# Performance work log

Measured on AMD Instinct MI355X. Metric: run time of the kernel, lower is better.

## Reference

```python
import jax, jax.numpy as jnp
import numpy as np

B, C, N = 512, 4, 24
D, H, L, DFF = 512, 8, 4, 2048
D2, D4 = D // 2, D // 4


def _ln(x, g, b):
    m = x.mean(-1, keepdims=True)
    v = ((x - m) ** 2).mean(-1, keepdims=True)
    return (x - m) / jnp.sqrt(v + 1e-5) * g + b


def setup_inputs():
    key = jax.random.key(0)
    ks = iter(jax.random.split(key, 80))
    def glorot(shape):
        fi, fo = shape[-2], shape[-1]
        return jax.random.normal(next(ks), shape, jnp.float32) * np.float32(np.sqrt(2.0 / (fi + fo)))
    z = lambda shape: jnp.zeros(shape, jnp.float32)
    o = lambda shape: jnp.ones(shape, jnp.float32)
    inp = {
        'encoded_features': jax.random.normal(next(ks), (B, C, D), jnp.float32),
        'original_keypoints': jax.random.normal(next(ks), (B, C, N, 2), jnp.float32),
        'depth_map': jax.random.uniform(next(ks), (B, C, N), jnp.float32),
        'occlusion_mask': jax.random.bernoulli(next(ks), 0.7, (B, C, N)),
        'kp_emb': jax.random.normal(next(ks), (N, D), jnp.float32) * 0.02,
        'view_emb': jax.random.normal(next(ks), (C, D), jnp.float32) * 0.02,
        'Wq': glorot((L, D, D)), 'bq': z((L, D)),
        'Wk': glorot((L, D, D)), 'bk': z((L, D)),
        'Wv': glorot((L, D, D)), 'bv': z((L, D)),
        'Wo': glorot((L, D, D)), 'bo': z((L, D)),
        'ln1_g': o((L, D)), 'ln1_b': z((L, D)),
        'ln2_g': o((L, D)), 'ln2_b': z((L, D)),
        'ffn_w1': glorot((L, D, DFF)), 'ffn_b1': z((L, DFF)),
        'ffn_w2': glorot((L, DFF, D)), 'ffn_b2': z((L, D)),
        'pred_w1': glorot((D, D2)), 'pred_b1': z((D2,)),
        'pred_w2': glorot((D2, D4)), 'pred_b2': z((D4,)),
        'pred_w3': glorot((D4, 2)), 'pred_b3': z((2,)),
        'de_w1': glorot((1, D4)), 'de_b1': z((D4,)),
        'de_w2': glorot((D4, D2)), 'de_b2': z((D2,)),
        'mp_w': glorot((D + D2, D)), 'mp_b': z((D,)),
        'dp_w1': glorot((D, D2)), 'dp_b1': z((D2,)),
        'dp_w2': glorot((D2, D4)), 'dp_b2': z((D4,)),
        'dp_w3': glorot((D4, 1)), 'dp_b3': z((1,)),
        'conf_w': glorot((D, 1)), 'conf_b': z((1,)),
    }
    return inp


def _forward(encoded_features, original_keypoints, depth_map, kp_emb, view_emb,
             Wq, bq, Wk, bk, Wv, bv, Wo, bo, ln1_g, ln1_b, ln2_g, ln2_b,
             ffn_w1, ffn_b1, ffn_w2, ffn_b2, pred_w1, pred_b1, pred_w2, pred_b2,
             pred_w3, pred_b3, de_w1, de_b1, de_w2, de_b2, mp_w, mp_b,
             dp_w1, dp_b1, dp_w2, dp_b2, dp_w3, dp_b3, conf_w, conf_b,
             occlusion_mask):
    occluded = ~occlusion_mask  # (B,C,N) True = needs inpainting
    # Vectorized replacement for the nested B*C ragged depth loop:
    # encode every depth scalar, masked mean over visible keypoints per (b,c).
    d_enc = jax.nn.gelu(depth_map[..., None] @ de_w1 + de_b1) @ de_w2 + de_b2  # (B,C,N,D2)
    vis = occlusion_mask[..., None].astype(jnp.float32)
    cnt = vis.sum(2)  # (B,C,1)
    depth_feat = jnp.where(cnt > 0, (d_enc * vis).sum(2) / jnp.maximum(cnt, 1.0), 0.0)
    # NOTE: faithful to source — `memory` is projected but the attention layers
    # consume encoded_features directly, so this is dead w.r.t. outputs.
    _memory = jnp.concatenate([encoded_features, depth_feat], -1) @ mp_w + mp_b

    # Dense query set over all (c,n); occluded positions selected at the end
    # (same math as the nonzero/gather version, jit-friendly fixed shapes).
    q = (view_emb[:, None, :] + kp_emb[None, :, :]).reshape(1, C * N, D)
    q = jnp.broadcast_to(q, (B, C * N, D))
    mem = encoded_features  # (B,C,D)
    dh = D // H
    scale = np.float32(1.0 / np.sqrt(dh))
    for l in range(L):  # post-LN cross-attention block (assumed standard block)
        qh = (q @ Wq[l] + bq[l]).reshape(B, C * N, H, dh)
        kh = (mem @ Wk[l] + bk[l]).reshape(B, C, H, dh)
        vh = (mem @ Wv[l] + bv[l]).reshape(B, C, H, dh)
        att = jax.nn.softmax(jnp.einsum('bqhd,bkhd->bhqk', qh, kh) * scale, axis=-1)
        attn_out = jnp.einsum('bhqk,bkhd->bqhd', att, vh).reshape(B, C * N, D) @ Wo[l] + bo[l]
        q = _ln(q + attn_out, ln1_g[l], ln1_b[l])
        f = jax.nn.gelu(q @ ffn_w1[l] + ffn_b1[l]) @ ffn_w2[l] + ffn_b2[l]
        q = _ln(q + f, ln2_g[l], ln2_b[l])

    feat = q  # (B, C*N, D)
    pred = jax.nn.gelu(feat @ pred_w1 + pred_b1)
    pred = jax.nn.gelu(pred @ pred_w2 + pred_b2) @ pred_w3 + pred_b3  # (B,CN,2)
    coords = jnp.where(occluded[..., None], pred.reshape(B, C, N, 2), original_keypoints)
    conf = jnp.where(occluded, jax.nn.sigmoid(feat @ conf_w + conf_b).reshape(B, C, N), 0.0)
    dp = jax.nn.gelu(feat @ dp_w1 + dp_b1)
    dp = jax.nn.softplus(jax.nn.gelu(dp @ dp_w2 + dp_b2) @ dp_w3 + dp_b3)
    depth = jnp.where(occluded, dp.reshape(B, C, N), 0.0)
    return coords, conf, depth


def reference(encoded_features, original_keypoints, depth_map, kp_emb, view_emb,
              Wq, bq, Wk, bk, Wv, bv, Wo, bo, ln1_g, ln1_b, ln2_g, ln2_b,
              ffn_w1, ffn_b1, ffn_w2, ffn_b2, pred_w1, pred_b1, pred_w2, pred_b2,
              pred_w3, pred_b3, de_w1, de_b1, de_w2, de_b2, mp_w, mp_b,
              dp_w1, dp_b1, dp_w2, dp_b2, dp_w3, dp_b3, conf_w, conf_b,
              occlusion_mask):
    return _forward(encoded_features, original_keypoints, depth_map, kp_emb, view_emb,
                    Wq, bq, Wk, bk, Wv, bv, Wo, bo, ln1_g, ln1_b, ln2_g, ln2_b,
                    ffn_w1, ffn_b1, ffn_w2, ffn_b2, pred_w1, pred_b1, pred_w2, pred_b2,
                    pred_w3, pred_b3, de_w1, de_b1, de_w2, de_b2, mp_w, mp_b,
                    dp_w1, dp_b1, dp_w2, dp_b2, dp_w3, dp_b3, conf_w, conf_b,
                    occlusion_mask)
```

## Files before the change

kernel.cpp:

```cpp
#include <hip/hip_runtime.h>
#include <hip/hip_bf16.h>
#include <stdint.h>

using bf16 = __hip_bfloat16;
typedef __attribute__((ext_vector_type(8))) short short8;
typedef __attribute__((ext_vector_type(4))) float f32x4;

#define GLD16(gptr, lptr) \
  __builtin_amdgcn_global_load_lds((const __attribute__((address_space(1))) void*)(gptr), \
                                   (__attribute__((address_space(3))) void*)(lptr), 16, 0, 0)

#define BARRIER_FENCED() do { \
  __builtin_amdgcn_s_barrier(); \
  asm volatile("" ::: "memory"); \
  __builtin_amdgcn_sched_barrier(0); \
} while (0)

__device__ __forceinline__ float b2f(bf16 h){ return __bfloat162float(h); }
__device__ __forceinline__ bf16  f2b(float f){ return __float2bfloat16(f); }
__device__ __forceinline__ float geluf(float x){
  float t2 = 1.5957691216057308f * (x + 0.044715f*x*x*x);
  return x / (1.0f + __expf(-t2));
}
__device__ __forceinline__ float wsum(float v){
  v += __shfl_xor(v,32); v += __shfl_xor(v,16); v += __shfl_xor(v,8);
  v += __shfl_xor(v,4);  v += __shfl_xor(v,2);  v += __shfl_xor(v,1);
  return v;
}

union BV { uint4 u; bf16 h[8]; };

template<int EPI>
__global__ __launch_bounds__(256, 2)
void gemm_bt(const bf16* __restrict__ A, int lda,
             const bf16* __restrict__ Bt,
             const float* __restrict__ bias,
             bf16* __restrict__ C, int ldc, int K)
{
  __shared__ __align__(16) bf16 smem[32768];
  const int tid  = threadIdx.x;
  const int wave = tid >> 6;
  const int lane = tid & 63;

  const int nwg = gridDim.x * gridDim.y;
  int bid = blockIdx.x + gridDim.x * blockIdx.y;
  if ((nwg & 7) == 0) bid = (bid & 7) * (nwg >> 3) + (bid >> 3);
  const int bx = bid % gridDim.x;
  const int by = bid / gridDim.x;
  const long mBlk = (long)by * 128;
  const int  nBlk = bx * 128;
  const int wm = (wave >> 1) * 64;
  const int wn = (wave & 1)  * 64;

  const int lr = lane >> 3;
  const int kc = ((lane & 7) ^ lr) << 3;
  const bf16* aS = A  + (mBlk + wave*32 + lr) * (long)lda + kc;
  const bf16* bS = Bt + (long)(nBlk + wave*32 + lr) * K   + kc;

  const int sA = lane >> 4;
  const int rA = wm + (lane & 15);
  const int rB = wn + (lane & 15);
  const int xA = rA & 7, xB = rB & 7;

  f32x4 acc[4][4];
  #pragma unroll
  for (int m=0;m<4;++m)
    #pragma unroll
    for (int n=0;n<4;++n)
      acc[m][n] = (f32x4){0.f,0.f,0.f,0.f};

  auto STAGE = [&](int b, int t) {
    bf16* sAl = smem + b*16384 + wave*2048;
    bf16* sBl = smem + b*16384 + 8192 + wave*2048;
    const int ko = t*64;
    #pragma unroll
    for (int c=0;c<4;++c) {
      GLD16(aS + (long)c*8*lda + ko, sAl + c*512);
      GLD16(bS + (long)c*8*K   + ko, sBl + c*512);
    }
  };
  auto COMPUTE = [&](int b) {
    const bf16* s = smem + b*16384;
    #pragma unroll
    for (int ks=0; ks<2; ++ks) {
      const int j = (ks<<2) + sA;
      short8 af[4], bfv[4];
      #pragma unroll
      for (int m=0;m<4;++m)
        af[m]  = *(const short8*)&s[(rA + m*16)*64 + ((j ^ xA) << 3)];
      #pragma unroll
      for (int n=0;n<4;++n)
        bfv[n] = *(const short8*)&s[8192 + (rB + n*16)*64 + ((j ^ xB) << 3)];
      #pragma unroll
      for (int m=0;m<4;++m)
        #pragma unroll
        for (int n=0;n<4;++n)
          acc[m][n] = __builtin_amdgcn_mfma_f32_16x16x32_bf16(af[m], bfv[n], acc[m][n], 0, 0, 0);
    }
  };

  STAGE(0, 0);
  asm volatile("s_waitcnt vmcnt(0)" ::: "memory");
  BARRIER_FENCED();

  const int nt = K >> 6;
  int cur = 0;
  for (int t = 0; t < nt - 1; ++t) {
    STAGE(cur ^ 1, t + 1);
    COMPUTE(cur);
    asm volatile("s_waitcnt vmcnt(0)" ::: "memory");
    BARRIER_FENCED();
    cur ^= 1;
  }
  COMPUTE(cur);

  __syncthreads();
  #pragma unroll
  for (int n=0;n<4;++n) {
    const int col = wn + n*16 + (lane & 15);
    float bi = bias[nBlk + col];
    #pragma unroll
    for (int m=0;m<4;++m) {
      #pragma unroll
      for (int j=0;j<4;++j) {
        float x = acc[m][n][j] + bi;
        if (EPI == 1) x = geluf(x);
        smem[(wm + m*16 + (lane>>4)*4 + j)*136 + col] = f2b(x);
      }
    }
  }
  __syncthreads();
  #pragma unroll
  for (int it=0; it<8; ++it) {
    int o = it*2048 + tid*8;
    int row = o >> 7, col = o & 127;
    uint4 v = *(const uint4*)&smem[row*136 + col];
    *(uint4*)&C[(mBlk + row)*(long)ldc + nBlk + col] = v;
  }
}

__global__ void transpose_w(const float* __restrict__ src, bf16* __restrict__ dst,
                            int N, long srcStride, long dstStride, int dstRowOff, int dstLd)
{
  __shared__ float t[32][33];
  src += (long)blockIdx.z * srcStride;
  dst += (long)blockIdx.z * dstStride;
  int n0 = blockIdx.x*32, k0 = blockIdx.y*32;
  int tx = threadIdx.x & 31, ty = threadIdx.x >> 5;
  #pragma unroll
  for (int r=0;r<4;++r) t[ty + r*8][tx] = src[(long)(k0+ty+r*8)*N + n0+tx];
  __syncthreads();
  #pragma unroll
  for (int r=0;r<4;++r)
    dst[(long)(dstRowOff + n0 + ty + r*8)*dstLd + k0 + tx] = f2b(t[tx][ty+r*8]);
}

__global__ void f32_to_bf16_k(const float* __restrict__ src, bf16* __restrict__ dst, long n)
{
  long i = ((long)blockIdx.x*256 + threadIdx.x) * 4;
  if (i + 3 < n) {
    float4 v = *(const float4*)(src + i);
    dst[i+0]=f2b(v.x); dst[i+1]=f2b(v.y); dst[i+2]=f2b(v.z); dst[i+3]=f2b(v.w);
  }
}

__global__ void concat2(float* __restrict__ dst, long dStride,
                        const float* __restrict__ a, long aStride, int na,
                        const float* __restrict__ b, long bStride, int nb)
{
  int z = blockIdx.y;
  int i = blockIdx.x*256 + threadIdx.x;
  if (i < na) dst[z*dStride + i] = a[z*aStride + i];
  else if (i < na + nb) dst[z*dStride + i] = b[z*bStride + (i - na)];
}

__global__ void init_q(const float* __restrict__ vw, const float* __restrict__ kp,
                       bf16* __restrict__ q)
{
  long gid = (long)blockIdx.x*256 + threadIdx.x;
  int b  = (int)(gid / 6144);
  int r  = (int)(gid % 6144);
  int cn = r >> 6;
  int d0 = (r & 63) * 8;
  int c = cn / 24, n = cn % 24;
  const float4* v4 = (const float4*)(vw + c*512 + d0);
  const float4* k4 = (const float4*)(kp + n*512 + d0);
  float4 va = v4[0], vb = v4[1], ka = k4[0], kb = k4[1];
  BV o;
  o.h[0]=f2b(va.x+ka.x); o.h[1]=f2b(va.y+ka.y); o.h[2]=f2b(va.z+ka.z); o.h[3]=f2b(va.w+ka.w);
  o.h[4]=f2b(vb.x+kb.x); o.h[5]=f2b(vb.y+kb.y); o.h[6]=f2b(vb.z+kb.z); o.h[7]=f2b(vb.w+kb.w);
  *(uint4*)(q + (long)b*49152 + cn*512 + d0) = o.u;
}

__global__ void add_ln(bf16* __restrict__ q, const bf16* __restrict__ res,
                       const float* __restrict__ g, const float* __restrict__ b)
{
  int row  = blockIdx.x*4 + (threadIdx.x >> 6);
  int lane = threadIdx.x & 63;
  long o = (long)row*512 + lane*8;
  BV Q, R;
  Q.u = *(const uint4*)(q + o);
  R.u = *(const uint4*)(res + o);
  float s[8]; float sum=0.f, sq=0.f;
  #pragma unroll
  for (int j=0;j<8;++j){ s[j] = b2f(Q.h[j]) + b2f(R.h[j]); sum += s[j]; sq += s[j]*s[j]; }
  sum = wsum(sum); sq = wsum(sq);
  float mean = sum * 0.001953125f;
  float var  = sq  * 0.001953125f - mean*mean;
  float rstd = rsqrtf(var + 1e-5f);
  const float4* g4 = (const float4*)(g + lane*8);
  const float4* b4 = (const float4*)(b + lane*8);
  float4 g0=g4[0], g1=g4[1], b0=b4[0], b1=b4[1];
  float gg[8] = {g0.x,g0.y,g0.z,g0.w,g1.x,g1.y,g1.z,g1.w};
  float bb[8] = {b0.x,b0.y,b0.z,b0.w,b1.x,b1.y,b1.z,b1.w};
  BV O;
  #pragma unroll
  for (int j=0;j<8;++j) O.h[j] = f2b((s[j]-mean)*rstd*gg[j] + bb[j]);
  *(uint4*)(q + o) = O.u;
}

__global__ void attn_k(bf16* __restrict__ qh, const bf16* __restrict__ kvh)
{
  int row  = blockIdx.x*4 + (threadIdx.x >> 6);
  int lane = threadIdx.x & 63;
  int b = row / 96;
  int d = (lane >> 3)*64 + (lane & 7)*8;
  BV Q;
  Q.u = *(const uint4*)(qh + (long)row*512 + d);
  float qf[8];
  #pragma unroll
  for (int j=0;j<8;++j) qf[j] = b2f(Q.h[j]);
  float s[4];
  #pragma unroll
  for (int c=0;c<4;++c){
    BV K; K.u = *(const uint4*)(kvh + (long)(b*4+c)*1024 + d);
    float p = 0.f;
    #pragma unroll
    for (int j=0;j<8;++j) p += qf[j]*b2f(K.h[j]);
    p += __shfl_xor(p,1); p += __shfl_xor(p,2); p += __shfl_xor(p,4);
    s[c] = p * 0.125f;
  }
  float mx = fmaxf(fmaxf(s[0],s[1]), fmaxf(s[2],s[3]));
  float e0=expf(s[0]-mx), e1=expf(s[1]-mx), e2=expf(s[2]-mx), e3=expf(s[3]-mx);
  float inv = 1.f/(e0+e1+e2+e3);
  float p4[4] = {e0*inv, e1*inv, e2*inv, e3*inv};
  float o[8] = {0,0,0,0,0,0,0,0};
  #pragma unroll
  for (int c=0;c<4;++c){
    BV V; V.u = *(const uint4*)(kvh + (long)(b*4+c)*1024 + 512 + d);
    #pragma unroll
    for (int j=0;j<8;++j) o[j] += p4[c]*b2f(V.h[j]);
  }
  BV O;
  #pragma unroll
  for (int j=0;j<8;++j) O.h[j] = f2b(o[j]);
  *(uint4*)(qh + (long)row*512 + d) = O.u;
}

__global__ void finalize_k(const bf16* __restrict__ feat, const bf16* __restrict__ p2dp2,
                           const float* __restrict__ cw, const float* __restrict__ cb,
                           const float* __restrict__ pw3, const float* __restrict__ pb3,
                           const float* __restrict__ dw3, const float* __restrict__ db3,
                           const int* __restrict__ occ, const float* __restrict__ okp,
                           float* __restrict__ out)
{
  int row  = blockIdx.x*4 + (threadIdx.x >> 6);
  int lane = threadIdx.x & 63;
  BV F; F.u = *(const uint4*)(feat + (long)row*512 + lane*8);
  const float4* c4 = (const float4*)(cw + lane*8);
  float4 ca = c4[0], cbv = c4[1];
  float cwv[8] = {ca.x,ca.y,ca.z,ca.w,cbv.x,cbv.y,cbv.z,cbv.w};
  float pc = 0.f;
  #pragma unroll
  for (int j=0;j<8;++j) pc += b2f(F.h[j]) * cwv[j];
  float sc = wsum(pc);
  int k = lane*2;
  long o2 = (long)row*256;
  float a0 = b2f(p2dp2[o2 + k]),       a1 = b2f(p2dp2[o2 + k + 1]);
  float d0 = b2f(p2dp2[o2 + 128 + k]), d1 = b2f(p2dp2[o2 + 128 + k + 1]);
  float sx = a0*pw3[k*2]   + a1*pw3[(k+1)*2];
  float sy = a0*pw3[k*2+1] + a1*pw3[(k+1)*2+1];
  float sd = d0*dw3[k]     + d1*dw3[k+1];
  sx = wsum(sx); sy = wsum(sy); sd = wsum(sd);
  if (lane == 0) {
    bool occl = (occ[row] == 0);
    out[row*2]   = occl ? (sx + pb3[0]) : okp[row*2];
    out[row*2+1] = occl ? (sy + pb3[1]) : okp[row*2+1];
    out[98304 + row] = occl ? 1.f/(1.f + expf(-(sc + cb[0]))) : 0.f;
    float dd = sd + db3[0];
    float sp = fmaxf(dd, 0.f) + log1pf(expf(-fabsf(dd)));
    out[147456 + row] = occl ? sp : 0.f;
  }
}

extern "C" void kernel_launch(void* const* d_in, const int* in_sizes, int n_in,
                              void* d_out, int out_size, void* d_ws, size_t ws_size,
                              hipStream_t stream)
{
  const float* enc  = (const float*)d_in[0];
  const float* okp  = (const float*)d_in[1];
  const int*   occ  = (const int*)  d_in[3];
  const float* kp   = (const float*)d_in[4];
  const float* vw   = (const float*)d_in[5];
  const float* Wq   = (const float*)d_in[6];
  const float* bq   = (const float*)d_in[7];
  const float* Wk   = (const float*)d_in[8];
  const float* bk   = (const float*)d_in[9];
  const float* Wv   = (const float*)d_in[10];
  const float* bv   = (const float*)d_in[11];
  const float* Wo   = (const float*)d_in[12];
  const float* bo   = (const float*)d_in[13];
  const float* ln1g = (const float*)d_in[14];
  const float* ln1b = (const float*)d_in[15];
  const float* ln2g = (const float*)d_in[16];
  const float* ln2b = (const float*)d_in[17];
  const float* fw1  = (const float*)d_in[18];
  const float* fb1  = (const float*)d_in[19];
  const float* fw2  = (const float*)d_in[20];
  const float* fb2  = (const float*)d_in[21];
  const float* pw1  = (const float*)d_in[22];
  const float* pb1  = (const float*)d_in[23];
  const float* pw2  = (const float*)d_in[24];
  const float* pb2  = (const float*)d_in[25];
  const float* pw3  = (const float*)d_in[26];
  const float* pb3  = (const float*)d_in[27];
  const float* dw1  = (const float*)d_in[34];
  const float* db1  = (const float*)d_in[35];
  const float* dw2  = (const float*)d_in[36];
  const float* db2  = (const float*)d_in[37];
  const float* dw3  = (const float*)d_in[38];
  const float* db3  = (const float*)d_in[39];
  const float* cw   = (const float*)d_in[40];
  const float* cb   = (const float*)d_in[41];

  uint8_t* base = (uint8_t*)d_ws;
  size_t off = 0;
  auto alloc = [&](size_t bytes) -> void* {
    void* p = base + off;
    off = (off + bytes + 255) & ~(size_t)255;
    return p;
  };
  bf16*  wqT  = (bf16*) alloc(4ull*512*512*2);
  bf16*  kvT  = (bf16*) alloc(4ull*1024*512*2);
  bf16*  woT  = (bf16*) alloc(4ull*512*512*2);
  bf16*  w1T  = (bf16*) alloc(4ull*2048*512*2);
  bf16*  w2T  = (bf16*) alloc(4ull*512*2048*2);
  bf16*  pd1T = (bf16*) alloc(512ull*512*2);
  bf16*  pw2T = (bf16*) alloc(128ull*256*2);
  bf16*  dw2T = (bf16*) alloc(128ull*256*2);
  float* bkvb = (float*)alloc(4ull*1024*4);
  float* pd1b = (float*)alloc(512ull*4);
  bf16*  mem16= (bf16*) alloc(2048ull*512*2);
  bf16*  kv16 = (bf16*) alloc(2048ull*1024*2);
  bf16*  q16  = (bf16*) alloc(49152ull*512*2);
  bf16*  bufQH= (bf16*) alloc(49152ull*512*2);
  size_t remainB = (ws_size > off) ? (ws_size - off) : 0;
  int chunkRows;
  if      (remainB >= 16384ull*2048*2 + 512) chunkRows = 16384;
  else if (remainB >= 12288ull*2048*2 + 512) chunkRows = 12288;
  else                                        chunkRows = 6144;
  bf16*  bufF1= (bf16*) alloc((size_t)chunkRows*2048*2);
  if (off > ws_size) return;
  const int nCh = 49152 / chunkRows;
  long woRows = (long)chunkRows * 4;
  if (woRows > 49152) woRows = 49152;
  const int nWo = (int)(49152 / woRows);

  dim3 T(256);
  transpose_w<<<dim3(16,16,4), T, 0, stream>>>(Wq,  wqT, 512, 512*512, 512*512, 0, 512);
  transpose_w<<<dim3(16,16,4), T, 0, stream>>>(Wk,  kvT, 512, 512*512, 1024*512, 0, 512);
  transpose_w<<<dim3(16,16,4), T, 0, stream>>>(Wv,  kvT, 512, 512*512, 1024*512, 512, 512);
  transpose_w<<<dim3(16,16,4), T, 0, stream>>>(Wo,  woT, 512, 512*512, 512*512, 0, 512);
  transpose_w<<<dim3(64,16,4), T, 0, stream>>>(fw1, w1T, 2048, 512*2048, 2048*512, 0, 512);
  transpose_w<<<dim3(16,64,4), T, 0, stream>>>(fw2, w2T, 512, 2048*512, 512*2048, 0, 2048);
  transpose_w<<<dim3(8,16,1),  T, 0, stream>>>(pw1, pd1T, 256, 0, 0, 0,   512);
  transpose_w<<<dim3(8,16,1),  T, 0, stream>>>(dw1, pd1T, 256, 0, 0, 256, 512);
  transpose_w<<<dim3(4,8,1),   T, 0, stream>>>(pw2, pw2T, 128, 0, 0, 0, 256);
  transpose_w<<<dim3(4,8,1),   T, 0, stream>>>(dw2, dw2T, 128, 0, 0, 0, 256);
  concat2<<<dim3(4,4), T, 0, stream>>>(bkvb, 1024, bk, 512, 512, bv, 512, 512);
  concat2<<<dim3(2,1), T, 0, stream>>>(pd1b, 512, pb1, 256, 256, db1, 256, 256);
  f32_to_bf16_k<<<dim3(1024), T, 0, stream>>>(enc, mem16, 2048ll*512);
  init_q<<<dim3(12288), T, 0, stream>>>(vw, kp, q16);

  for (int l = 0; l < 4; ++l) {
    gemm_bt<0><<<dim3(4,384), T, 0, stream>>>(q16, 512, wqT + l*262144, bq + l*512, bufQH, 512, 512);
    gemm_bt<0><<<dim3(8,16),  T, 0, stream>>>(mem16, 512, kvT + l*524288, bkvb + l*1024, kv16, 1024, 512);
    attn_k<<<dim3(12288), T, 0, stream>>>(bufQH, kv16);
    for (int c = 0; c < nWo; ++c) {
      gemm_bt<0><<<dim3(4, (int)(woRows>>7)), T, 0, stream>>>(bufQH + (long)c*woRows*512, 512,
                                                woT + l*262144, bo + l*512, bufF1, 512, 512);
      add_ln<<<dim3((int)(woRows>>2)), T, 0, stream>>>(q16 + (long)c*woRows*512, bufF1,
                                           ln1g + l*512, ln1b + l*512);
    }
    for (int c = 0; c < nCh; ++c) {
      gemm_bt<1><<<dim3(16, chunkRows>>7), T, 0, stream>>>(q16 + (long)c*chunkRows*512, 512,
                                                w1T + l*1048576, fb1 + l*2048, bufF1, 2048, 512);
      gemm_bt<0><<<dim3(4, chunkRows>>7),  T, 0, stream>>>(bufF1, 2048,
                                                w2T + l*1048576, fb2 + l*512,
                                                bufQH + (long)c*chunkRows*512, 512, 2048);
      add_ln<<<dim3(chunkRows>>2), T, 0, stream>>>(q16 + (long)c*chunkRows*512,
                                           bufQH + (long)c*chunkRows*512,
                                           ln2g + l*512, ln2b + l*512);
    }
  }

  gemm_bt<1><<<dim3(4,384), T, 0, stream>>>(q16, 512, pd1T, pd1b, bufQH, 512, 512);
  gemm_bt<1><<<dim3(1,384), T, 0, stream>>>(bufQH, 512, pw2T, pb2, bufF1, 256, 256);
  gemm_bt<1><<<dim3(1,384), T, 0, stream>>>(bufQH + 256, 512, dw2T, db2, bufF1 + 128, 256, 256);
  finalize_k<<<dim3(12288), T, 0, stream>>>(q16, bufF1, cw, cb, pw3, pb3, dw3, db3,
                                            occ, okp, (float*)d_out);
}
```

Before: 1.711 ms.

## Single-buffer GEMM for higher occupancy; dedupe layer-0 Q projection across batch

```diff
diff --git a/kernel.cpp b/kernel.cpp
--- a/kernel.cpp
+++ b/kernel.cpp
@@ -9,12 +9,6 @@
 #define GLD16(gptr, lptr) \
   __builtin_amdgcn_global_load_lds((const __attribute__((address_space(1))) void*)(gptr), \
                                    (__attribute__((address_space(3))) void*)(lptr), 16, 0, 0)
-
-#define BARRIER_FENCED() do { \
-  __builtin_amdgcn_s_barrier(); \
-  asm volatile("" ::: "memory"); \
-  __builtin_amdgcn_sched_barrier(0); \
-} while (0)
 
 __device__ __forceinline__ float b2f(bf16 h){ return __bfloat162float(h); }
 __device__ __forceinline__ bf16  f2b(float f){ return __float2bfloat16(f); }
@@ -31,13 +25,13 @@
 union BV { uint4 u; bf16 h[8]; };
 
 template<int EPI>
-__global__ __launch_bounds__(256, 2)
+__global__ __launch_bounds__(256, 4)
 void gemm_bt(const bf16* __restrict__ A, int lda,
              const bf16* __restrict__ Bt,
              const float* __restrict__ bias,
              bf16* __restrict__ C, int ldc, int K)
 {
-  __shared__ __align__(16) bf16 smem[32768];
+  __shared__ __align__(16) bf16 smem[17408];
   const int tid  = threadIdx.x;
   const int wave = tid >> 6;
   const int lane = tid & 63;
@@ -69,52 +63,38 @@
     for (int n=0;n<4;++n)
       acc[m][n] = (f32x4){0.f,0.f,0.f,0.f};
 
-  auto STAGE = [&](int b, int t) {
-    bf16* sAl = smem + b*16384 + wave*2048;
-    bf16* sBl = smem + b*16384 + 8192 + wave*2048;
-    const int ko = t*64;
-    #pragma unroll
-    for (int c=0;c<4;++c) {
-      GLD16(aS + (long)c*8*lda + ko, sAl + c*512);
-      GLD16(bS + (long)c*8*K   + ko, sBl + c*512);
-    }
-  };
-  auto COMPUTE = [&](int b) {
-    const bf16* s = smem + b*16384;
+  const int nt = K >> 6;
+  for (int t = 0; t < nt; ++t) {
+    {
+      bf16* sAl = smem + wave*2048;
+      bf16* sBl = smem + 8192 + wave*2048;
+      const int ko = t*64;
+      #pragma unroll
+      for (int c=0;c<4;++c) {
+        GLD16(aS + (long)c*8*lda + ko, sAl + c*512);
+        GLD16(bS + (long)c*8*K   + ko, sBl + c*512);
+      }
+    }
+    __syncthreads();
     #pragma unroll
     for (int ks=0; ks<2; ++ks) {
       const int j = (ks<<2) + sA;
       short8 af[4], bfv[4];
       #pragma unroll
       for (int m=0;m<4;++m)
-        af[m]  = *(const short8*)&s[(rA + m*16)*64 + ((j ^ xA) << 3)];
+        af[m]  = *(const short8*)&smem[(rA + m*16)*64 + ((j ^ xA) << 3)];
       #pragma unroll
       for (int n=0;n<4;++n)
-        bfv[n] = *(const short8*)&s[8192 + (rB + n*16)*64 + ((j ^ xB) << 3)];
+        bfv[n] = *(const short8*)&smem[8192 + (rB + n*16)*64 + ((j ^ xB) << 3)];
       #pragma unroll
       for (int m=0;m<4;++m)
         #pragma unroll
         for (int n=0;n<4;++n)
           acc[m][n] = __builtin_amdgcn_mfma_f32_16x16x32_bf16(af[m], bfv[n], acc[m][n], 0, 0, 0);
     }
-  };
-
-  STAGE(0, 0);
-  asm volatile("s_waitcnt vmcnt(0)" ::: "memory");
-  BARRIER_FENCED();
-
-  const int nt = K >> 6;
-  int cur = 0;
-  for (int t = 0; t < nt - 1; ++t) {
-    STAGE(cur ^ 1, t + 1);
-    COMPUTE(cur);
-    asm volatile("s_waitcnt vmcnt(0)" ::: "memory");
-    BARRIER_FENCED();
-    cur ^= 1;
-  }
-  COMPUTE(cur);
-
-  __syncthreads();
+    __syncthreads();
+  }
+
   #pragma unroll
   for (int n=0;n<4;++n) {
     const int col = wn + n*16 + (lane & 15);
@@ -192,6 +172,22 @@
   *(uint4*)(q + (long)b*49152 + cn*512 + d0) = o.u;
 }
 
+__global__ void init_q96(const float* __restrict__ vw, const float* __restrict__ kp,
+                         bf16* __restrict__ q96)
+{
+  int gid = blockIdx.x*256 + threadIdx.x;
+  int cn = gid >> 6;
+  int d0 = (gid & 63) * 8;
+  int c = cn / 24, n = cn % 24;
+  const float4* v4 = (const float4*)(vw + c*512 + d0);
+  const float4* k4 = (const float4*)(kp + n*512 + d0);
+  float4 va = v4[0], vb = v4[1], ka = k4[0], kb = k4[1];
+  BV o;
+  o.h[0]=f2b(va.x+ka.x); o.h[1]=f2b(va.y+ka.y); o.h[2]=f2b(va.z+ka.z); o.h[3]=f2b(va.w+ka.w);
+  o.h[4]=f2b(vb.x+kb.x); o.h[5]=f2b(vb.y+kb.y); o.h[6]=f2b(vb.z+kb.z); o.h[7]=f2b(vb.w+kb.w);
+  *(uint4*)(q96 + (long)cn*512 + d0) = o.u;
+}
+
 __global__ void add_ln(bf16* __restrict__ q, const bf16* __restrict__ res,
                        const float* __restrict__ g, const float* __restrict__ b)
 {
@@ -219,14 +215,16 @@
   *(uint4*)(q + o) = O.u;
 }
 
-__global__ void attn_k(bf16* __restrict__ qh, const bf16* __restrict__ kvh)
+__global__ void attn_k(const bf16* __restrict__ qsrc, int qMod,
+                       const bf16* __restrict__ kvh, bf16* __restrict__ dst)
 {
   int row  = blockIdx.x*4 + (threadIdx.x >> 6);
   int lane = threadIdx.x & 63;
   int b = row / 96;
+  int qRow = qMod ? (row % qMod) : row;
   int d = (lane >> 3)*64 + (lane & 7)*8;
   BV Q;
-  Q.u = *(const uint4*)(qh + (long)row*512 + d);
+  Q.u = *(const uint4*)(qsrc + (long)qRow*512 + d);
   float qf[8];
   #pragma unroll
   for (int j=0;j<8;++j) qf[j] = b2f(Q.h[j]);
@@ -254,7 +252,7 @@
   BV O;
   #pragma unroll
   for (int j=0;j<8;++j) O.h[j] = f2b(o[j]);
-  *(uint4*)(qh + (long)row*512 + d) = O.u;
+  *(uint4*)(dst + (long)row*512 + d) = O.u;
 }
 
 __global__ void finalize_k(const bf16* __restrict__ feat, const bf16* __restrict__ p2dp2,
@@ -352,6 +350,8 @@
   float* pd1b = (float*)alloc(512ull*4);
   bf16*  mem16= (bf16*) alloc(2048ull*512*2);
   bf16*  kv16 = (bf16*) alloc(2048ull*1024*2);
+  bf16*  q96  = (bf16*) alloc(128ull*512*2);
+  bf16*  qh96 = (bf16*) alloc(128ull*512*2);
   bf16*  q16  = (bf16*) alloc(49152ull*512*2);
   bf16*  bufQH= (bf16*) alloc(49152ull*512*2);
   size_t remainB = (ws_size > off) ? (ws_size - off) : 0;
@@ -381,11 +381,17 @@
   concat2<<<dim3(2,1), T, 0, stream>>>(pd1b, 512, pb1, 256, 256, db1, 256, 256);
   f32_to_bf16_k<<<dim3(1024), T, 0, stream>>>(enc, mem16, 2048ll*512);
   init_q<<<dim3(12288), T, 0, stream>>>(vw, kp, q16);
+  init_q96<<<dim3(24), T, 0, stream>>>(vw, kp, q96);
 
   for (int l = 0; l < 4; ++l) {
-    gemm_bt<0><<<dim3(4,384), T, 0, stream>>>(q16, 512, wqT + l*262144, bq + l*512, bufQH, 512, 512);
+    if (l == 0) {
+      gemm_bt<0><<<dim3(4,1), T, 0, stream>>>(q96, 512, wqT, bq, qh96, 512, 512);
+    } else {
+      gemm_bt<0><<<dim3(4,384), T, 0, stream>>>(q16, 512, wqT + l*262144, bq + l*512, bufQH, 512, 512);
+    }
     gemm_bt<0><<<dim3(8,16),  T, 0, stream>>>(mem16, 512, kvT + l*524288, bkvb + l*1024, kv16, 1024, 512);
-    attn_k<<<dim3(12288), T, 0, stream>>>(bufQH, kv16);
+    if (l == 0) attn_k<<<dim3(12288), T, 0, stream>>>(qh96, 96, kv16, bufQH);
+    else        attn_k<<<dim3(12288), T, 0, stream>>>(bufQH, 0, kv16, bufQH);
     for (int c = 0; c < nWo; ++c) {
       gemm_bt<0><<<dim3(4, (int)(woRows>>7)), T, 0, stream>>>(bufQH + (long)c*woRows*512, 512,
                                                 woT + l*262144, bo + l*512, bufF1, 512, 512);
```

Result: faster. 1.653 ms (-3.4%).
